# Performance work log

Measured on AMD Instinct MI355X. Metric: run time of the kernel, lower is better.

Reference implementation:

```python
import jax, jax.numpy as jnp
from jax import lax
import numpy as np

T, B, V, H = 256, 32, 4712, 500

def _lstm_scan(xs, h0, c0, Wih, Whh, bih, bhh):
    # xs: (T, B, in); PyTorch gate order i, f, g, o
    def step(carry, x):
        h, c = carry
        g = x @ Wih.T + bih + h @ Whh.T + bhh  # (B, 4H)
        i, f, gg, o = jnp.split(g, 4, axis=-1)
        c = jax.nn.sigmoid(f) * c + jax.nn.sigmoid(i) * jnp.tanh(gg)
        h = jax.nn.sigmoid(o) * jnp.tanh(c)
        return (h, c), h
    (h, c), hs = lax.scan(step, (h0, c0), xs)
    return (h, c), hs


def setup_inputs() -> dict:
    key = jax.random.key(0)
    ks = jax.random.split(key, 12)
    s = 0.05
    inp = {
        "sequence": jax.random.normal(ks[0], (T, B, V), jnp.float32),
        "numbered_seq": jax.random.randint(ks[1], (T, B), 0, V),
        "enc_Wih": jax.random.normal(ks[2], (4 * H, V), jnp.float32) * s,
        "enc_Whh": jax.random.normal(ks[3], (4 * H, H), jnp.float32) * s,
        "enc_bih": jax.random.normal(ks[4], (4 * H,), jnp.float32) * s,
        "enc_bhh": jax.random.normal(ks[5], (4 * H,), jnp.float32) * s,
        "dec_Wih": jax.random.normal(ks[6], (4 * H, V), jnp.float32) * s,
        "dec_Whh": jax.random.normal(ks[7], (4 * H, H), jnp.float32) * s,
        "dec_bih": jax.random.normal(ks[8], (4 * H,), jnp.float32) * s,
        "dec_bhh": jax.random.normal(ks[9], (4 * H,), jnp.float32) * s,
        "out_W": jax.random.normal(ks[10], (V, H), jnp.float32) * s,
        "out_b": jax.random.normal(ks[11], (V,), jnp.float32) * s,
    }
    return inp


def reference(sequence, numbered_seq, enc_Wih, enc_Whh, enc_bih, enc_bhh,
              dec_Wih, dec_Whh, dec_bih, dec_bhh, out_W, out_b):
    seq_len, batch = sequence.shape[0], sequence.shape[1]
    h0 = jnp.zeros((batch, H), sequence.dtype)
    c0 = jnp.zeros((batch, H), sequence.dtype)
    # Encoder consumes timesteps T-1, T-2, ..., 1 (index 0 excluded)
    enc_inputs = sequence[-1:0:-1]
    (h, c), _ = _lstm_scan(enc_inputs, h0, c0, enc_Wih, enc_Whh, enc_bih, enc_bhh)
    # Decoder with full teacher forcing: inputs are sequence[0:T-1]
    (_, _), dec_h = _lstm_scan(sequence[:-1], h, c, dec_Wih, dec_Whh, dec_bih, dec_bhh)
    logits = dec_h @ out_W.T + out_b                  # (T-1, B, V)
    all_outputs = jnp.concatenate([sequence[:1], logits], axis=0)  # (T, B, V)
    # masked NLL; all lengths == seq_len so mask is all-ones
    logp = jax.nn.log_softmax(all_outputs, axis=-1)
    nll = -jnp.take_along_axis(logp, numbered_seq[..., None], axis=-1)[..., 0]
    loss = nll.sum() / (seq_len * batch)
    return loss
```

## Files before the change

### kernel.cpp

```cpp
#include <hip/hip_runtime.h>
#include <math.h>

typedef unsigned long long ull;
typedef __attribute__((ext_vector_type(8))) short s16x8;
typedef __attribute__((ext_vector_type(8))) unsigned short u16x8;
typedef __attribute__((ext_vector_type(4))) float f32x4;
typedef __attribute__((ext_vector_type(4))) unsigned int u32x4;

#define TT 256
#define BB 32
#define VV 4712
#define HH 500
#define FOURH 2000
#define MPRE 8160

#define OFF_DECPRE 16320000
#define OFF_HR     33100000
#define OFF_DECH   38449920
#define OFF_NLL    42561920
#define RING_SLOTS 16384

__device__ __forceinline__ unsigned short f2b(float f) {
  unsigned int b = __float_as_uint(f);
  b = b + 0x7fffu + ((b >> 16) & 1u);
  return (unsigned short)(b >> 16);
}

__device__ __forceinline__ unsigned cvtpk(float lo, float hi) {
  unsigned r;
  asm("v_cvt_pk_bf16_f32 %0, %1, %2" : "=v"(r) : "v"(lo), "v"(hi));
  return r;
}

__device__ __forceinline__ float fsig(float x) {
  return 1.0f / (1.0f + __expf(-x));
}
__device__ __forceinline__ float ftanh(float x) {
  return 1.0f - 2.0f / (__expf(2.0f * x) + 1.0f);
}

__global__ __launch_bounds__(512) void gemm_bf16_256(
    const float* __restrict__ A, int lda,
    const float* __restrict__ W, int ldw, int rowmapW,
    int bias_mode, const float* __restrict__ b0, const float* __restrict__ b1,
    float* __restrict__ C, int ldc, int M, int N, int K,
    int ntiles, int swz) {
  __shared__ __align__(16) unsigned short As[2][256 * 40];
  __shared__ __align__(16) unsigned short Bs[2][256 * 40];

  const int tid = threadIdx.x;
  const int lane = tid & 63, wid = tid >> 6;
  const int wm = wid >> 2, wn = wid & 3;
  const int row16 = lane & 15, kq = lane >> 4;
  int mt, nt;
  if (swz) { mt = blockIdx.x & 7; nt = blockIdx.x >> 3; }
  else     { nt = blockIdx.x % ntiles; mt = blockIdx.x / ntiles; }
  const int m0 = mt * 256, n0 = nt * 256;

  const int sr = tid >> 1;
  const int ks = (tid & 1) << 4;
  int am = m0 + sr; if (am >= M) am = M - 1;
  const float* arow = A + (long)am * lda;
  int nn = n0 + sr; if (nn >= N) nn = N - 1;
  int rn = nn;
  if (rowmapW) { int t = nn >> 5, b = nn & 31; rn = ((255 - t) << 5) + b; }
  const float* wrow = W + (long)rn * ldw;

  f32x4 acc[8][4];
#pragma unroll
  for (int i = 0; i < 8; ++i)
#pragma unroll
    for (int j = 0; j < 4; ++j) acc[i][j] = (f32x4){0.f, 0.f, 0.f, 0.f};

  float4 av[4], wv[4];

#define LOAD_TILE(kt_)                                                      \
  do {                                                                      \
    const int kb_ = (kt_) * 32 + ks;                                        \
    _Pragma("unroll")                                                       \
    for (int q = 0; q < 4; ++q) {                                           \
      const int k_ = kb_ + q * 4;     \
      if (k_ < K) {                                                         \
        av[q] = *(const float4*)(arow + k_);                                \
        wv[q] = *(const float4*)(wrow + k_);                                \
      } else {                                                              \
        av[q] = make_float4(0.f, 0.f, 0.f, 0.f);                            \
        wv[q] = make_float4(0.f, 0.f, 0.f, 0.f);                            \
      }                                                                     \
    }                                                                       \
  } while (0)

#define CVT_STORE(bq_)                                                      \
  do {                                                                      \
    const u32x4 qa0 = {cvtpk(av[0].x, av[0].y), cvtpk(av[0].z, av[0].w),    \
                       cvtpk(av[1].x, av[1].y), cvtpk(av[1].z, av[1].w)};   \
    const u32x4 qa1 = {cvtpk(av[2].x, av[2].y), cvtpk(av[2].z, av[2].w),    \
                       cvtpk(av[3].x, av[3].y), cvtpk(av[3].z, av[3].w)};   \
    const u32x4 qw0 = {cvtpk(wv[0].x, wv[0].y), cvtpk(wv[0].z, wv[0].w),    \
                       cvtpk(wv[1].x, wv[1].y), cvtpk(wv[1].z, wv[1].w)};   \
    const u32x4 qw1 = {cvtpk(wv[2].x, wv[2].y), cvtpk(wv[2].z, wv[2].w),    \
                       cvtpk(wv[3].x, wv[3].y), cvtpk(wv[3].z, wv[3].w)};   \
    *(u32x4*)&As[bq_][sr * 40 + ks + 0] = qa0;                              \
    *(u32x4*)&As[bq_][sr * 40 + ks + 8] = qa1;                              \
    *(u32x4*)&Bs[bq_][sr * 40 + ks + 0] = qw0;                              \
    *(u32x4*)&Bs[bq_][sr * 40 + ks + 8] = qw1;                              \
  } while (0)

  LOAD_TILE(0);
  CVT_STORE(0);
  __syncthreads();

  const int KT = (K + 31) >> 5;
  for (int kt = 0; kt < KT; ++kt) {
    const int cur = kt & 1;
    const bool more = (kt + 1 < KT);
    if (more) LOAD_TILE(kt + 1);

    s16x8 afrag[8], bfrag[4];
#pragma unroll
    for (int i = 0; i < 8; ++i)
      afrag[i] = *(const s16x8*)&As[cur][(wm * 128 + i * 16 + row16) * 40 + kq * 8];
#pragma unroll
    for (int j = 0; j < 4; ++j)
      bfrag[j] = *(const s16x8*)&Bs[cur][(wn * 64 + j * 16 + row16) * 40 + kq * 8];
#pragma unroll
    for (int i = 0; i < 8; ++i)
#pragma unroll
      for (int j = 0; j < 4; ++j)
        acc[i][j] = __builtin_amdgcn_mfma_f32_16x16x32_bf16(
            afrag[i], bfrag[j], acc[i][j], 0, 0, 0);

    if (more) {
      CVT_STORE(cur ^ 1);
      __syncthreads();
    }
  }
#undef LOAD_TILE
#undef CVT_STORE

#pragma unroll
  for (int i = 0; i < 8; ++i) {
    const int rbase = m0 + wm * 128 + i * 16 + kq * 4;
#pragma unroll
    for (int r = 0; r < 4; ++r) {
      const int mrow = rbase + r;
      if (mrow < M) {
        const float rb = (bias_mode == 1) ? (b0[mrow] + b1[mrow]) : 0.0f;
        float* crow = C + (long)mrow * ldc;
#pragma unroll
        for (int j = 0; j < 4; ++j) {
          const int col = n0 + wn * 64 + j * 16 + row16;
          if (col < N) {
            float v = acc[i][j][r] + rb;
            if (bias_mode == 0 && b0) v += b0[col];
            crow[col] = v;
          }
        }
      }
    }
  }
}

#define PITCH_H 544
__global__ __launch_bounds__(256) void lstm_rec(
    const float* __restrict__ enc_preT, const float* __restrict__ dec_preT,
    const float* __restrict__ enc_Whh, const float* __restrict__ dec_Whh,
    ull* __restrict__ hring, float* __restrict__ dec_h) {
  __shared__ __align__(16) unsigned short hb16[2][4 * PITCH_H];

  const int tid = threadIdx.x;
  const int lane = tid & 63, w = tid >> 6;
  const int kq = lane >> 4;
  const int X = blockIdx.x & 31, Y = blockIdx.x >> 5;
  const int u0 = X * 16, b0 = Y * 4;
  const int gbase = Y * 2048;

  const int arr = lane & 15;
  const int ag  = arr & 3;
  const int au  = u0 + w * 4 + (arr >> 2);
  const bool auok = (au < 500);

  const int c    = lane & 15;
  const int uout = u0 + w * 4 + kq;
  const bool act = (c < 4) && (uout < 500);
  long preoff[4];
#pragma unroll
  for (int g = 0; g < 4; ++g)
    preoff[g] = (long)(g * 500 + (act ? uout : 0)) * MPRE + b0 + (act ? c : 0);

  if (tid < 352) {
    const int bq = tid / 176, rr = tid % 176;
    const int cc = rr / 44, k = 500 + rr % 44;
    hb16[bq][cc * PITCH_H + k] = 0;
  }
  __syncthreads();

  float creg = 0.0f;

  const float* pres[2] = {enc_preT, dec_preT};
  const float* whhs[2] = {enc_Whh, dec_Whh};
  unsigned step = 0;

  for (int ph = 0; ph < 2; ++ph) {
    const float* pre = pres[ph];
    const float* Whh = whhs[ph];

    s16x8 afrag[16];
    {
      const float* wrow = Whh + (long)(ag * 500 + (auok ? au : 0)) * 500;
#pragma unroll
      for (int ch = 0; ch < 16; ++ch) {
        const int k0 = ch * 32 + kq * 8;
        float4 v0 = make_float4(0.f, 0.f, 0.f, 0.f);
        float4 v1 = make_float4(0.f, 0.f, 0.f, 0.f);
        if (auok && k0 < 500)     v0 = *(const float4*)(wrow + k0);
        if (auok && k0 + 4 < 500) v1 = *(const float4*)(wrow + k0 + 4);
        const u16x8 p = {f2b(v0.x), f2b(v0.y), f2b(v0.z), f2b(v0.w),
                         f2b(v1.x), f2b(v1.y), f2b(v1.z), f2b(v1.w)};
        afrag[ch] = (s16x8)p;
      }
    }

    for (int t = 0; t < 255; ++t) {
      ++step;
      const unsigned want = step - 1;
      const int buf = step & 1;
      const ull* rring = hring + (ull)((step - 1) % 3) * RING_SLOTS + gbase;
      ull* wring = hring + (ull)(step % 3) * RING_SLOTS + gbase;

      float pv[4];
#pragma unroll
      for (int g = 0; g < 4; ++g) pv[g] = pre[preoff[g] + t * 32];

      unsigned pend = (tid < 208) ? 0xffu : 0x7fu;
      while (pend) {
        unsigned np = pend;
#pragma unroll
        for (int j = 0; j < 8; ++j) {
          if (np & (1u << j)) {
            const int s = tid + j * 256;
            const ull v = __hip_atomic_load(&rring[s], __ATOMIC_RELAXED,
                                            __HIP_MEMORY_SCOPE_AGENT);
            if ((unsigned)(v >> 32) >= want) {
              hb16[buf][(s & 3) * PITCH_H + (s >> 2)] =
                  f2b(__uint_as_float((unsigned)(v & 0xffffffffu)));
              np &= ~(1u << j);
            }
          }
        }
        pend = np;
        if (pend) __builtin_amdgcn_s_sleep(1);
      }
      __syncthreads();

      f32x4 acc = (f32x4){0.f, 0.f, 0.f, 0.f};
      const unsigned short* hbase = &hb16[buf][(c & 3) * PITCH_H + kq * 8];
#pragma unroll
      for (int ch = 0; ch < 16; ++ch) {
        const s16x8 bfrag = *(const s16x8*)(hbase + ch * 32);
        acc = __builtin_amdgcn_mfma_f32_16x16x32_bf16(afrag[ch], bfrag, acc,
                                                      0, 0, 0);
      }

      if (act) {
        const float iv = acc[0] + pv[0];
        const float fv = acc[1] + pv[1];
        const float gv = acc[2] + pv[2];
        const float ov = acc[3] + pv[3];
        const float cn = fsig(fv) * creg + fsig(iv) * ftanh(gv);
        const float hn = fsig(ov) * ftanh(cn);
        creg = cn;
        __hip_atomic_store(&wring[(uout << 2) + c],
                           ((ull)step << 32) | __float_as_uint(hn),
                           __ATOMIC_RELAXED, __HIP_MEMORY_SCOPE_AGENT);
        if (ph == 1)
          dec_h[(long)(t * 32 + b0 + c) * 500 + uout] = hn;
      }
    }
  }
}

__device__ __forceinline__ float wave_max(float v) {
#pragma unroll
  for (int o = 32; o > 0; o >>= 1) v = fmaxf(v, __shfl_xor(v, o, 64));
  return v;
}
__device__ __forceinline__ float wave_sum(float v) {
#pragma unroll
  for (int o = 32; o > 0; o >>= 1) v += __shfl_xor(v, o, 64);
  return v;
}

__global__ __launch_bounds__(256) void loss_rows(
    const float* __restrict__ seq, const float* __restrict__ logits,
    const int* __restrict__ nseq, float* __restrict__ nll) {
  __shared__ float sm[8];
  const int r = blockIdx.x, tid = threadIdx.x;
  const int t = r >> 5, b = r & 31;
  const float* row = (t == 0) ? (seq + (long)b * VV)
                              : (logits + (long)((t - 1) * 32 + b) * VV);
  float m = -INFINITY;
  for (int c = tid; c < 1178; c += 256) {
    float4 v = *(const float4*)&row[c * 4];
    m = fmaxf(m, fmaxf(fmaxf(v.x, v.y), fmaxf(v.z, v.w)));
  }
  m = wave_max(m);
  const int wid = tid >> 6;
  if ((tid & 63) == 0) sm[wid] = m;
  __syncthreads();
  const float M4 = fmaxf(fmaxf(sm[0], sm[1]), fmaxf(sm[2], sm[3]));
  float s = 0.0f;
  for (int c = tid; c < 1178; c += 256) {
    float4 v = *(const float4*)&row[c * 4];
    s += expf(v.x - M4) + expf(v.y - M4) + expf(v.z - M4) + expf(v.w - M4);
  }
  s = wave_sum(s);
  if ((tid & 63) == 0) sm[4 + wid] = s;
  __syncthreads();
  if (tid == 0) {
    const float S = sm[4] + sm[5] + sm[6] + sm[7];
    const int tgt = nseq[(t << 5) + b];
    nll[r] = M4 + logf(S) - row[tgt];
  }
}

__global__ __launch_bounds__(256) void final_reduce(
    const float* __restrict__ nll, float* __restrict__ out) {
  __shared__ float sm[4];
  float s = 0.0f;
  for (int c = threadIdx.x; c < 8192; c += 256) s += nll[c];
  s = wave_sum(s);
  if ((threadIdx.x & 63) == 0) sm[threadIdx.x >> 6] = s;
  __syncthreads();
  if (threadIdx.x == 0) out[0] = (sm[0] + sm[1] + sm[2] + sm[3]) * (1.0f / 8192.0f);
}

extern "C" void kernel_launch(void* const* d_in, const int* in_sizes, int n_in,
                              void* d_out, int out_size, void* d_ws, size_t ws_size,
                              hipStream_t stream) {
  (void)in_sizes; (void)n_in; (void)out_size; (void)ws_size;
  const float* seq  = (const float*)d_in[0];
  const int* nseq   = (const int*)d_in[1];
  const float* eWih = (const float*)d_in[2];
  const float* eWhh = (const float*)d_in[3];
  const float* ebih = (const float*)d_in[4];
  const float* ebhh = (const float*)d_in[5];
  const float* dWih = (const float*)d_in[6];
  const float* dWhh = (const float*)d_in[7];
  const float* dbih = (const float*)d_in[8];
  const float* dbhh = (const float*)d_in[9];
  const float* oW   = (const float*)d_in[10];
  const float* ob   = (const float*)d_in[11];

  float* wsf = (float*)d_ws;
  float* logits   = wsf;
  float* enc_preT = wsf;
  float* dec_preT = wsf + OFF_DECPRE;
  ull*   hring    = (ull*)(wsf + OFF_HR);
  float* dec_h    = wsf + OFF_DECH;
  float* nll      = wsf + OFF_NLL;

  hipMemsetAsync(hring, 0, 3 * RING_SLOTS * sizeof(ull), stream);

  gemm_bf16_256<<<dim3(256), dim3(512), 0, stream>>>(
      eWih, VV, seq, VV, 1, 1, ebih, ebhh,
      enc_preT, MPRE, FOURH, MPRE, VV, 32, 1);
  gemm_bf16_256<<<dim3(256), dim3(512), 0, stream>>>(
      dWih, VV, seq, VV, 0, 1, dbih, dbhh,
      dec_preT, MPRE, FOURH, MPRE, VV, 32, 1);
  lstm_rec<<<dim3(256), dim3(256), 0, stream>>>(enc_preT, dec_preT, eWhh, dWhh,
                                                hring, dec_h);
  gemm_bf16_256<<<dim3(608), dim3(512), 0, stream>>>(
      dec_h, HH, oW, HH, 0, 0, ob, nullptr,
      logits, VV, MPRE, VV, HH, 19, 0);
  loss_rows<<<dim3(8192), dim3(256), 0, stream>>>(seq, logits, nseq, nll);
  final_reduce<<<dim3(1), dim3(256), 0, stream>>>(nll, (float*)d_out);
}
```

Measured before the change: 3.232 ms.

## Replace per-element tagged ring polling with per-block step flags in LSTM recurrence

Cross-block exchange of hidden states in the persistent LSTM kernel changes from 64-bit slots tagged with the step number to plain 32-bit values plus one flag per producer block. Each block now spins on 32 flags using only 32 threads, then reads the ring once without retries; producers publish their flag with a release store after a block barrier. This removes the heavy per-element polling traffic and halves the ring data size. In exchange it adds extra barriers and a serialized data-then-flag publish per step, and its correctness relies on relaxed agent-scope loads seeing the data after the flag, since no explicit acquire is used.

```diff
diff --git a/kernel.cpp b/kernel.cpp
--- a/kernel.cpp
+++ b/kernel.cpp
@@ -18,7 +18,7 @@
 #define OFF_HR     33100000
 #define OFF_DECH   38449920
 #define OFF_NLL    42561920
-#define RING_SLOTS 16384
+#define RING_U32 16384
 
 __device__ __forceinline__ unsigned short f2b(float f) {
   unsigned int b = __float_as_uint(f);
@@ -165,7 +165,8 @@
 __global__ __launch_bounds__(256) void lstm_rec(
     const float* __restrict__ enc_preT, const float* __restrict__ dec_preT,
     const float* __restrict__ enc_Whh, const float* __restrict__ dec_Whh,
-    ull* __restrict__ hring, float* __restrict__ dec_h) {
+    unsigned* __restrict__ hring, unsigned* __restrict__ sent,
+    float* __restrict__ dec_h) {
   __shared__ __align__(16) unsigned short hb16[2][4 * PITCH_H];
 
   const int tid = threadIdx.x;
@@ -174,6 +175,7 @@
   const int X = blockIdx.x & 31, Y = blockIdx.x >> 5;
   const int u0 = X * 16, b0 = Y * 4;
   const int gbase = Y * 2048;
+  unsigned* gsent = sent + Y * 32;
 
   const int arr = lane & 15;
   const int ag  = arr & 3;
@@ -225,31 +227,28 @@
       ++step;
       const unsigned want = step - 1;
       const int buf = step & 1;
-      const ull* rring = hring + (ull)((step - 1) % 3) * RING_SLOTS + gbase;
-      ull* wring = hring + (ull)(step % 3) * RING_SLOTS + gbase;
+      const unsigned* rring = hring + (ull)((step - 1) % 3) * RING_U32 + gbase;
+      unsigned* wring = hring + (ull)(step % 3) * RING_U32 + gbase;
 
       float pv[4];
 #pragma unroll
       for (int g = 0; g < 4; ++g) pv[g] = pre[preoff[g] + t * 32];
 
-      unsigned pend = (tid < 208) ? 0xffu : 0x7fu;
-      while (pend) {
-        unsigned np = pend;
-#pragma unroll
-        for (int j = 0; j < 8; ++j) {
-          if (np & (1u << j)) {
-            const int s = tid + j * 256;
-            const ull v = __hip_atomic_load(&rring[s], __ATOMIC_RELAXED,
-                                            __HIP_MEMORY_SCOPE_AGENT);
-            if ((unsigned)(v >> 32) >= want) {
-              hb16[buf][(s & 3) * PITCH_H + (s >> 2)] =
-                  f2b(__uint_as_float((unsigned)(v & 0xffffffffu)));
-              np &= ~(1u << j);
-            }
-          }
+      if (tid < 32) {
+        while (__hip_atomic_load(&gsent[tid], __ATOMIC_RELAXED,
+                                 __HIP_MEMORY_SCOPE_AGENT) < want) {
+          __builtin_amdgcn_s_sleep(1);
         }
-        pend = np;
-        if (pend) __builtin_amdgcn_s_sleep(1);
+      }
+      __syncthreads();
+
+#pragma unroll
+      for (int j = 0; j < 8; ++j) {
+        const int s = tid + j * 256;
+        const unsigned v = __hip_atomic_load(&rring[s], __ATOMIC_RELAXED,
+                                             __HIP_MEMORY_SCOPE_AGENT);
+        if (s < 2000)
+          hb16[buf][(s & 3) * PITCH_H + (s >> 2)] = f2b(__uint_as_float(v));
       }
       __syncthreads();
 
@@ -270,12 +269,16 @@
         const float cn = fsig(fv) * creg + fsig(iv) * ftanh(gv);
         const float hn = fsig(ov) * ftanh(cn);
         creg = cn;
-        __hip_atomic_store(&wring[(uout << 2) + c],
-                           ((ull)step << 32) | __float_as_uint(hn),
+        __hip_atomic_store(&wring[(uout << 2) + c], __float_as_uint(hn),
                            __ATOMIC_RELAXED, __HIP_MEMORY_SCOPE_AGENT);
         if (ph == 1)
           dec_h[(long)(t * 32 + b0 + c) * 500 + uout] = hn;
       }
+
+      __syncthreads();
+      if (tid == 0)
+        __hip_atomic_store(&gsent[X], step, __ATOMIC_RELEASE,
+                           __HIP_MEMORY_SCOPE_AGENT);
     }
   }
 }
@@ -356,11 +359,12 @@
   float* logits   = wsf;
   float* enc_preT = wsf;
   float* dec_preT = wsf + OFF_DECPRE;
-  ull*   hring    = (ull*)(wsf + OFF_HR);
+  unsigned* hring = (unsigned*)(wsf + OFF_HR);
+  unsigned* sent  = hring + 3 * RING_U32;
   float* dec_h    = wsf + OFF_DECH;
   float* nll      = wsf + OFF_NLL;
 
-  hipMemsetAsync(hring, 0, 3 * RING_SLOTS * sizeof(ull), stream);
+  hipMemsetAsync(hring, 0, (3 * RING_U32 + 256) * sizeof(unsigned), stream);
 
   gemm_bf16_256<<<dim3(256), dim3(512), 0, stream>>>(
       eWih, VV, seq, VV, 1, 1, ebih, ebhh,
@@ -369,7 +373,7 @@
       dWih, VV, seq, VV, 0, 1, dbih, dbhh,
       dec_preT, MPRE, FOURH, MPRE, VV, 32, 1);
   lstm_rec<<<dim3(256), dim3(256), 0, stream>>>(enc_preT, dec_preT, eWhh, dWhh,
-                                                hring, dec_h);
+                                                hring, sent, dec_h);
   gemm_bf16_256<<<dim3(608), dim3(512), 0, stream>>>(
       dec_h, HH, oW, HH, 0, 0, ob, nullptr,
       logits, VV, MPRE, VV, HH, 19, 0);
```

Result: slower. 5.288 ms (+63.6%).
